# Kernel optimization log

Measured on AMD Instinct MI355X. Metric: run time of the kernel, lower is better.

## Reference

```python
import jax, jax.numpy as jnp
import numpy as np

D_MODEL = 1024
NUM_HEADS = 16
D_K = D_MODEL // NUM_HEADS


def setup_inputs() -> dict:
    key = jax.random.key(0)
    ks = jax.random.split(key, 12)
    B, S = 1, 4096
    s = 1.0 / np.sqrt(D_MODEL)
    inp = {
        'query': jax.random.normal(ks[0], (B, S, D_MODEL), jnp.float32),
        'key': jax.random.normal(ks[1], (B, S, D_MODEL), jnp.float32),
        'value': jax.random.normal(ks[2], (B, S, D_MODEL), jnp.float32),
        'W_q': jax.random.normal(ks[3], (D_MODEL, D_MODEL), jnp.float32) * s,
        'b_q': jnp.zeros((D_MODEL,), jnp.float32),
        'W_k': jax.random.normal(ks[4], (D_MODEL, D_MODEL), jnp.float32) * s,
        'b_k': jnp.zeros((D_MODEL,), jnp.float32),
        'W_v': jax.random.normal(ks[5], (D_MODEL, D_MODEL), jnp.float32) * s,
        'b_v': jnp.zeros((D_MODEL,), jnp.float32),
        'W_o': jax.random.normal(ks[6], (D_MODEL, D_MODEL), jnp.float32) * s,
        'b_o': jnp.zeros((D_MODEL,), jnp.float32),
    }
    return inp


def reference(query, key, value, W_q, b_q, W_k, b_k, W_v, b_v, W_o, b_o):
    B, S, _ = query.shape
    # torch nn.Linear: y = x @ W.T + b
    Q = query @ W_q.T + b_q
    K = key @ W_k.T + b_k
    V = value @ W_v.T + b_v
    # (B, S, H, d_k) -> (B, H, S, d_k)
    Q = Q.reshape(B, S, NUM_HEADS, D_K).transpose(0, 2, 1, 3)
    K = K.reshape(B, S, NUM_HEADS, D_K).transpose(0, 2, 1, 3)
    V = V.reshape(B, S, NUM_HEADS, D_K).transpose(0, 2, 1, 3)
    scale = 1.0 / jnp.sqrt(jnp.asarray(D_K, Q.dtype))
    qk = jnp.einsum('bhqd,bhkd->bhqk', Q, K) * scale  # [B,H,S,S]
    attn = jax.nn.softmax(qk, axis=-1)
    out = jnp.einsum('bhqk,bhkd->bhqd', attn, V)
    out = out.transpose(0, 2, 1, 3).reshape(B, S, D_MODEL)
    return out @ W_o.T + b_o
```

## Files before the change

### kernel.cpp

```cpp
#include <hip/hip_runtime.h>
#include <cstdint>
#include <cstddef>

typedef __bf16 bf16_t;
typedef _Float16 f16_t;
typedef __attribute__((ext_vector_type(8))) __bf16 bf16x8;
typedef __attribute__((ext_vector_type(4))) __bf16 bf16x4;
typedef __attribute__((ext_vector_type(2))) __bf16 bf16x2;
typedef __attribute__((ext_vector_type(8))) _Float16 f16x8;
typedef __attribute__((ext_vector_type(2))) _Float16 f16x2;
typedef __attribute__((ext_vector_type(4))) float floatx4;
typedef __attribute__((ext_vector_type(16))) float floatx16;

#define S_LEN 4096
#define DM 1024
#define NH 16
#define DKH 64
#define NSPLIT 4
#define KT_PER (S_LEN / 64 / NSPLIT)

#define QSCALE 0.1803368801111601f

__device__ __forceinline__ void async_b128(void* lds, const void* g) {
    __builtin_amdgcn_global_load_lds(
        (__attribute__((address_space(1))) void*)(uintptr_t)g,
        (__attribute__((address_space(3))) void*)lds,
        16, 0, 0);
}

__device__ __forceinline__ void fence_all() { __builtin_amdgcn_s_waitcnt(0); }

__device__ __forceinline__ floatx4 mfma16(bf16x8 a, bf16x8 b, floatx4 c) {
    return __builtin_amdgcn_mfma_f32_16x16x32_bf16(a, b, c, 0, 0, 0);
}
__device__ __forceinline__ floatx16 mfma32(bf16x8 a, bf16x8 b, floatx16 c) {
    return __builtin_amdgcn_mfma_f32_32x32x16_bf16(a, b, c, 0, 0, 0);
}
__device__ __forceinline__ int f2i(float x) { return __builtin_bit_cast(int, x); }
__device__ __forceinline__ float i2f(int x) { return __builtin_bit_cast(float, x); }
__device__ __forceinline__ int p2i(bf16x2 x) { return __builtin_bit_cast(int, x); }
__device__ __forceinline__ bf16x2 i2p(int x) { return __builtin_bit_cast(bf16x2, x); }

__global__ __launch_bounds__(256) void convert_all_kernel(
    const float* __restrict__ q, const float* __restrict__ k,
    const float* __restrict__ v, const float* __restrict__ wqf,
    const float* __restrict__ wkf, const float* __restrict__ wvf,
    const float* __restrict__ wof, bf16_t* __restrict__ dst_in,
    bf16_t* __restrict__ dst_w) {
    const size_t i = ((size_t)blockIdx.x * 256 + threadIdx.x) * 4;
    const float* s;
    bf16_t* d;
    size_t off;
    if (i < 12582912) {
        const int r = (int)(i >> 22);
        s = (r == 0) ? q : (r == 1) ? k : v;
        off = i & 4194303;
        d = dst_in + (size_t)r * 4194304 + off;
    } else {
        const size_t j = i - 12582912;
        const int r = (int)(j >> 20);
        s = (r == 0) ? wqf : (r == 1) ? wkf : (r == 2) ? wvf : wof;
        off = j & 1048575;
        d = dst_w + (size_t)r * 1048576 + off;
    }
    const floatx4 val = *(const floatx4*)(s + off);
    bf16x4 o;
    o[0] = (bf16_t)val[0]; o[1] = (bf16_t)val[1];
    o[2] = (bf16_t)val[2]; o[3] = (bf16_t)val[3];
    *(bf16x4*)d = o;
}

template <int BN, typename OutT>
__device__ __forceinline__ void gemm_bt_body(const bf16_t* __restrict__ A,
                                             const bf16_t* __restrict__ B,
                                             const float* __restrict__ bias,
                                             OutT* __restrict__ C, float oscale) {
    constexpr int K = 1024, N = 1024;
    constexpr int NT = BN / 32;
    __shared__ bf16_t As[2][128 * 32];
    __shared__ bf16_t Bs[2][BN * 32];
    const int tid = threadIdx.x;
    const int wid = tid >> 6, lane = tid & 63;
    const int quad = lane >> 4, l16 = lane & 15;
    const int m0 = blockIdx.x * 128, n0 = blockIdx.y * BN;
    const int wm = (wid & 1) * 64, wn = (wid >> 1) * (BN / 2);

    floatx4 acc[4][NT] = {};

    auto stage = [&](int buf, int k0) {
#pragma unroll
        for (int i = 0; i < 2; ++i) {
            const int c = (i << 8) + tid;
            const int row = c >> 2;
            const int ko = (c & 3) << 3;
            const int lb = ((i << 8) + (wid << 6)) << 3;
            async_b128(&As[buf][lb], A + (size_t)(m0 + row) * K + k0 + ko);
        }
#pragma unroll
        for (int i = 0; i < BN / 64; ++i) {
            const int c = (i << 8) + tid;
            const int row = c >> 2;
            const int ko = (c & 3) << 3;
            const int lb = ((i << 8) + (wid << 6)) << 3;
            async_b128(&Bs[buf][lb], B + (size_t)(n0 + row) * K + k0 + ko);
        }
    };

    stage(0, 0);
    for (int step = 0; step < K / 32; ++step) {
        const int buf = step & 1;
        fence_all();
        __syncthreads();
        if (step + 1 < K / 32) stage(buf ^ 1, (step + 1) * 32);

        bf16x8 af[4], bfr[NT];
#pragma unroll
        for (int t = 0; t < 4; ++t)
            af[t] = *(const bf16x8*)&As[buf][(wm + t * 16 + l16) * 32 + quad * 8];
#pragma unroll
        for (int t = 0; t < NT; ++t)
            bfr[t] = *(const bf16x8*)&Bs[buf][(wn + t * 16 + l16) * 32 + quad * 8];
#pragma unroll
        for (int mt = 0; mt < 4; ++mt)
#pragma unroll
            for (int nt = 0; nt < NT; ++nt)
                acc[mt][nt] = mfma16(af[mt], bfr[nt], acc[mt][nt]);
    }

#pragma unroll
    for (int mt = 0; mt < 4; ++mt)
#pragma unroll
        for (int nt = 0; nt < NT; ++nt) {
            const int col = n0 + wn + nt * 16 + l16;
            const float bv = bias[col];
#pragma unroll
            for (int r = 0; r < 4; ++r) {
                const int row = m0 + wm + mt * 16 + quad * 4 + r;
                C[(size_t)row * N + col] = (OutT)((acc[mt][nt][r] + bv) * oscale);
            }
        }
}

__global__ __launch_bounds__(256) void gemm_qkv_kernel(
    const bf16_t* __restrict__ qx, const bf16_t* __restrict__ kx,
    const bf16_t* __restrict__ vx, const bf16_t* __restrict__ wq,
    const bf16_t* __restrict__ wk, const bf16_t* __restrict__ wv,
    const float* __restrict__ bq, const float* __restrict__ bk,
    const float* __restrict__ bv, bf16_t* __restrict__ Qp,
    bf16_t* __restrict__ Kp, bf16_t* __restrict__ Vp) {
    const int z = blockIdx.z;
    const bf16_t* A = (z == 0) ? qx : (z == 1) ? kx : vx;
    const bf16_t* B = (z == 0) ? wq : (z == 1) ? wk : wv;
    const float* bias = (z == 0) ? bq : (z == 1) ? bk : bv;
    bf16_t* C = (z == 0) ? Qp : (z == 1) ? Kp : Vp;
    gemm_bt_body<128, bf16_t>(A, B, bias, C, (z == 0) ? QSCALE : 1.0f);
}

__global__ __launch_bounds__(256) void gemm_out_kernel(
    const bf16_t* __restrict__ AO, const bf16_t* __restrict__ wo,
    const float* __restrict__ bo, float* __restrict__ out) {
    gemm_bt_body<64, float>(AO, wo, bo, out, 1.0f);
}

__global__ __launch_bounds__(256) void transpose_kernel(
    const bf16_t* __restrict__ in, bf16_t* __restrict__ out) {
    __shared__ bf16_t tile[64][65];
    const int tx = threadIdx.x & 63;
    const int ty = threadIdx.x >> 6;
    const int c0 = blockIdx.x * 64;
    const int r0 = blockIdx.y * 64;
#pragma unroll
    for (int i = 0; i < 16; ++i) {
        const int r = ty + i * 4;
        tile[r][tx] = in[(size_t)(r0 + r) * DM + c0 + tx];
    }
    __syncthreads();
#pragma unroll
    for (int i = 0; i < 16; ++i) {
        const int c = ty + i * 4;
        out[(size_t)(c0 + c) * S_LEN + r0 + tx] = tile[tx][c];
    }
}

__global__ __launch_bounds__(256, 2) void flash_kernel(
    const bf16_t* __restrict__ Q, const bf16_t* __restrict__ K,
    const bf16_t* __restrict__ Vt, f16_t* __restrict__ Opart,
    float* __restrict__ Lpart) {
    __shared__ bf16_t smem[16384];
    bf16_t* Ks = smem;
    bf16_t* Vs = smem + 8192;

    const int tid = threadIdx.x;
    const int wave = tid >> 6, lane = tid & 63;
    const int h32 = lane >> 5, c = lane & 31;
    const int head = blockIdx.x;
    const int sp = blockIdx.z;
    const int qbase = blockIdx.y * 256 + wave * 64;
    const int kv0 = sp * (S_LEN / NSPLIT);

    bf16x8 Qf[2][4];
#pragma unroll
    for (int nt = 0; nt < 2; ++nt)
#pragma unroll
        for (int s = 0; s < 4; ++s)
            Qf[nt][s] = *(const bf16x8*)(Q + (size_t)(qbase + nt * 32 + c) * DM +
                                         head * DKH + s * 16 + h32 * 8);

    floatx16 oa[2][2] = {};
    floatx4 la[2] = {};

    const bf16_t* kptr = K + (size_t)(kv0 + lane) * DM + head * DKH + wave * 16;
    const bf16_t* vptr = Vt + (size_t)(head * DKH + lane) * S_LEN + kv0 + wave * 16;
    bf16_t* ksl = Ks + wave * 1024;
    bf16_t* vsl = Vs + wave * 1024;

    async_b128(ksl, kptr);       async_b128(ksl + 512, kptr + 8);
    async_b128(vsl, vptr);       async_b128(vsl + 512, vptr + 8);
    kptr += 64 * DM; vptr += 64;

    for (int kt = 0; kt < KT_PER; ++kt) {
        const int buf = kt & 1;
        fence_all();
        __syncthreads();
        if (kt + 1 < KT_PER) {
            bf16_t* kd = ksl + (buf ^ 1) * 4096;
            bf16_t* vd = vsl + (buf ^ 1) * 4096;
            async_b128(kd, kptr);     async_b128(kd + 512, kptr + 8);
            async_b128(vd, vptr);     async_b128(vd + 512, vptr + 8);
            kptr += 64 * DM; vptr += 64;
        }

        bf16x8 Kf[2][4];
#pragma unroll
        for (int mt = 0; mt < 2; ++mt)
#pragma unroll
            for (int s = 0; s < 4; ++s)
                Kf[mt][s] = *(const bf16x8*)&Ks[buf * 4096 + ((2 * s + h32) * 64 + mt * 32 + c) * 8];

        floatx16 sc[2][2] = {};
#pragma unroll
        for (int s = 0; s < 4; ++s)
#pragma unroll
            for (int mt = 0; mt < 2; ++mt)
#pragma unroll
                for (int nt = 0; nt < 2; ++nt)
                    sc[mt][nt] = mfma32(Kf[mt][s], Qf[nt][s], sc[mt][nt]);

        bf16x8 Vf[2][4];
#pragma unroll
        for (int dt = 0; dt < 2; ++dt)
#pragma unroll
            for (int s = 0; s < 4; ++s)
                Vf[dt][s] = *(const bf16x8*)&Vs[buf * 4096 + ((2 * s + h32) * 64 + dt * 32 + c) * 8];

#pragma unroll
        for (int nt = 0; nt < 2; ++nt) {
            bf16x2 pk[2][8];
#pragma unroll
            for (int mt = 0; mt < 2; ++mt)
#pragma unroll
                for (int rr = 0; rr < 8; ++rr) {
                    const float p0 = __builtin_amdgcn_exp2f(sc[mt][nt][2 * rr] - 3.0f);
                    const float p1 = __builtin_amdgcn_exp2f(sc[mt][nt][2 * rr + 1] - 3.0f);
                    la[nt][(2 * rr) & 3] += p0;
                    la[nt][(2 * rr + 1) & 3] += p1;
                    bf16x2 w; w[0] = (bf16_t)p0; w[1] = (bf16_t)p1;
                    pk[mt][rr] = w;
                }
#pragma unroll
            for (int s = 0; s < 4; ++s) {
                const int a = s >> 1, b4 = (s & 1) * 4;
                const bf16x2 r0 = h32 ? pk[a][b4 + 2] : pk[a][b4 + 0];
                const bf16x2 r1 = h32 ? pk[a][b4 + 3] : pk[a][b4 + 1];
                const bf16x2 s0 = h32 ? pk[a][b4 + 0] : pk[a][b4 + 2];
                const bf16x2 s1 = h32 ? pk[a][b4 + 1] : pk[a][b4 + 3];
                const bf16x2 x0 = i2p(__shfl_xor(p2i(s0), 32));
                const bf16x2 x1 = i2p(__shfl_xor(p2i(s1), 32));
                union { bf16x8 v; bf16x2 d[4]; } P;
                P.d[0] = h32 ? x0 : r0;
                P.d[1] = h32 ? x1 : r1;
                P.d[2] = h32 ? r0 : x0;
                P.d[3] = h32 ? r1 : x1;
                oa[0][nt] = mfma32(Vf[0][s], P.v, oa[0][nt]);
                oa[1][nt] = mfma32(Vf[1][s], P.v, oa[1][nt]);
            }
        }
    }

#pragma unroll
    for (int nt = 0; nt < 2; ++nt) {
        float t = la[nt][0] + la[nt][1] + la[nt][2] + la[nt][3];
        t += i2f(__shfl_xor(f2i(t), 32));
        if (h32 == 0)
            Lpart[(size_t)(sp * NH + head) * S_LEN + qbase + nt * 32 + c] = t;
    }

    fence_all();
    __syncthreads();
    f16_t* ot = (f16_t*)smem + wave * (32 * 72);
#pragma unroll
    for (int nt = 0; nt < 2; ++nt) {
#pragma unroll
        for (int dt = 0; dt < 2; ++dt)
#pragma unroll
            for (int rr = 0; rr < 8; ++rr) {
                const int d0 = dt * 32 + ((2 * rr) & 3) + 8 * (rr >> 1) + 4 * h32;
                f16x2 w;
                w[0] = (f16_t)oa[dt][nt][2 * rr];
                w[1] = (f16_t)oa[dt][nt][2 * rr + 1];
                *(f16x2*)&ot[c * 72 + d0] = w;
            }
        fence_all();
        __syncthreads();
        const int r = lane & 31;
#pragma unroll
        for (int j = 0; j < 4; ++j) {
            const f16x8 v = *(const f16x8*)&ot[r * 72 + h32 * 32 + j * 8];
            *(f16x8*)(Opart + ((size_t)sp * S_LEN + qbase + nt * 32 + r) * DM +
                      head * DKH + h32 * 32 + j * 8) = v;
        }
        fence_all();
        __syncthreads();
    }
}

__global__ __launch_bounds__(256) void reduce_kernel(
    const f16_t* __restrict__ Op, const float* __restrict__ Lp,
    bf16_t* __restrict__ AO) {
    const size_t f = ((size_t)blockIdx.x * 256 + threadIdx.x) * 8;
    const int q = (int)(f >> 10);
    const int h = (int)((f & 1023) >> 6);
    float l = 0.f;
#pragma unroll
    for (int sp = 0; sp < NSPLIT; ++sp)
        l += Lp[(size_t)(sp * NH + h) * S_LEN + q];
    const float inv = 1.0f / l;
    float s[8] = {};
#pragma unroll
    for (int sp = 0; sp < NSPLIT; ++sp) {
        const f16x8 v = *(const f16x8*)(Op + (size_t)sp * (S_LEN * DM) + f);
#pragma unroll
        for (int j = 0; j < 8; ++j) s[j] += (float)v[j];
    }
    bf16x8 o;
#pragma unroll
    for (int j = 0; j < 8; ++j) o[j] = (bf16_t)(s[j] * inv);
    *(bf16x8*)(AO + f) = o;
}

extern "C" void kernel_launch(void* const* d_in, const int* in_sizes, int n_in,
                              void* d_out, int out_size, void* d_ws, size_t ws_size,
                              hipStream_t stream) {
    const float* q  = (const float*)d_in[0];
    const float* k  = (const float*)d_in[1];
    const float* v  = (const float*)d_in[2];
    const float* Wq = (const float*)d_in[3];
    const float* bq = (const float*)d_in[4];
    const float* Wk = (const float*)d_in[5];
    const float* bk = (const float*)d_in[6];
    const float* Wv = (const float*)d_in[7];
    const float* bv = (const float*)d_in[8];
    const float* Wo = (const float*)d_in[9];
    const float* bo = (const float*)d_in[10];
    float* out = (float*)d_out;

    bf16_t* ws = (bf16_t*)d_ws;
    bf16_t* qx = ws;
    bf16_t* kx = qx + 4194304;
    bf16_t* vx = kx + 4194304;
    bf16_t* Vp = vx + 4194304;
    f16_t*  Opart = (f16_t*)ws;
    bf16_t* wq = Vp + 4194304;
    bf16_t* wk = wq + 1048576;
    bf16_t* wv = wk + 1048576;
    bf16_t* wo = wv + 1048576;
    bf16_t* Qp = wo + 1048576;
    bf16_t* Kp = Qp + 4194304;
    bf16_t* Vt = Kp + 4194304;
    bf16_t* AO = Vt + 4194304;
    float*  Lpart = (float*)(AO + 4194304);

    convert_all_kernel<<<dim3(16384), 256, 0, stream>>>(q, k, v, Wq, Wk, Wv, Wo,
                                                        qx, wq);
    gemm_qkv_kernel<<<dim3(32, 8, 3), 256, 0, stream>>>(qx, kx, vx, wq, wk, wv,
                                                        bq, bk, bv, Qp, Kp, Vp);
    transpose_kernel<<<dim3(16, 64), 256, 0, stream>>>(Vp, Vt);
    flash_kernel<<<dim3(16, 16, NSPLIT), 256, 0, stream>>>(Qp, Kp, Vt, Opart, Lpart);
    reduce_kernel<<<dim3(2048), 256, 0, stream>>>(Opart, Lpart, AO);
    gemm_out_kernel<<<dim3(32, 16), 256, 0, stream>>>(AO, wo, bo, out);
    (void)in_sizes; (void)n_in; (void)out_size; (void)ws_size;
}
```

Measured before the change: 284.1 us.

## Fuse V transpose into QKV GEMM epilogue and rebalance flash attention tiling

```diff
diff --git a/kernel.cpp b/kernel.cpp
--- a/kernel.cpp
+++ b/kernel.cpp
@@ -16,7 +16,7 @@
 #define DM 1024
 #define NH 16
 #define DKH 64
-#define NSPLIT 4
+#define NSPLIT 2
 #define KT_PER (S_LEN / 64 / NSPLIT)
 
 #define QSCALE 0.1803368801111601f
@@ -70,7 +70,7 @@
     *(bf16x4*)d = o;
 }
 
-template <int BN, typename OutT>
+template <int BN, typename OutT, bool TR>
 __device__ __forceinline__ void gemm_bt_body(const bf16_t* __restrict__ A,
                                              const bf16_t* __restrict__ B,
                                              const float* __restrict__ bias,
@@ -133,10 +133,19 @@
         for (int nt = 0; nt < NT; ++nt) {
             const int col = n0 + wn + nt * 16 + l16;
             const float bv = bias[col];
-#pragma unroll
-            for (int r = 0; r < 4; ++r) {
-                const int row = m0 + wm + mt * 16 + quad * 4 + r;
-                C[(size_t)row * N + col] = (OutT)((acc[mt][nt][r] + bv) * oscale);
+            if (TR) {
+                bf16x4 o4;
+#pragma unroll
+                for (int r = 0; r < 4; ++r)
+                    o4[r] = (bf16_t)((acc[mt][nt][r] + bv) * oscale);
+                *(bf16x4*)((bf16_t*)C + (size_t)col * S_LEN +
+                           (m0 + wm + mt * 16 + quad * 4)) = o4;
+            } else {
+#pragma unroll
+                for (int r = 0; r < 4; ++r) {
+                    const int row = m0 + wm + mt * 16 + quad * 4 + r;
+                    C[(size_t)row * N + col] = (OutT)((acc[mt][nt][r] + bv) * oscale);
+                }
             }
         }
 }
@@ -146,40 +155,24 @@
     const bf16_t* __restrict__ vx, const bf16_t* __restrict__ wq,
     const bf16_t* __restrict__ wk, const bf16_t* __restrict__ wv,
     const float* __restrict__ bq, const float* __restrict__ bk,
-    const float* __restrict__ bv, bf16_t* __restrict__ Qp,
-    bf16_t* __restrict__ Kp, bf16_t* __restrict__ Vp) {
+    const float* __restrict__ bvv, bf16_t* __restrict__ Qp,
+    bf16_t* __restrict__ Kp, bf16_t* __restrict__ Vt) {
     const int z = blockIdx.z;
-    const bf16_t* A = (z == 0) ? qx : (z == 1) ? kx : vx;
-    const bf16_t* B = (z == 0) ? wq : (z == 1) ? wk : wv;
-    const float* bias = (z == 0) ? bq : (z == 1) ? bk : bv;
-    bf16_t* C = (z == 0) ? Qp : (z == 1) ? Kp : Vp;
-    gemm_bt_body<128, bf16_t>(A, B, bias, C, (z == 0) ? QSCALE : 1.0f);
+    if (z == 2) {
+        gemm_bt_body<128, bf16_t, true>(vx, wv, bvv, Vt, 1.0f);
+    } else {
+        const bf16_t* A = (z == 0) ? qx : kx;
+        const bf16_t* B = (z == 0) ? wq : wk;
+        const float* bias = (z == 0) ? bq : bk;
+        bf16_t* C = (z == 0) ? Qp : Kp;
+        gemm_bt_body<128, bf16_t, false>(A, B, bias, C, (z == 0) ? QSCALE : 1.0f);
+    }
 }
 
 __global__ __launch_bounds__(256) void gemm_out_kernel(
     const bf16_t* __restrict__ AO, const bf16_t* __restrict__ wo,
     const float* __restrict__ bo, float* __restrict__ out) {
-    gemm_bt_body<64, float>(AO, wo, bo, out, 1.0f);
-}
-
-__global__ __launch_bounds__(256) void transpose_kernel(
-    const bf16_t* __restrict__ in, bf16_t* __restrict__ out) {
-    __shared__ bf16_t tile[64][65];
-    const int tx = threadIdx.x & 63;
-    const int ty = threadIdx.x >> 6;
-    const int c0 = blockIdx.x * 64;
-    const int r0 = blockIdx.y * 64;
-#pragma unroll
-    for (int i = 0; i < 16; ++i) {
-        const int r = ty + i * 4;
-        tile[r][tx] = in[(size_t)(r0 + r) * DM + c0 + tx];
-    }
-    __syncthreads();
-#pragma unroll
-    for (int i = 0; i < 16; ++i) {
-        const int c = ty + i * 4;
-        out[(size_t)(c0 + c) * S_LEN + r0 + tx] = tile[tx][c];
-    }
+    gemm_bt_body<64, float, false>(AO, wo, bo, out, 1.0f);
 }
 
 __global__ __launch_bounds__(256, 2) void flash_kernel(
@@ -195,19 +188,17 @@
     const int h32 = lane >> 5, c = lane & 31;
     const int head = blockIdx.x;
     const int sp = blockIdx.z;
-    const int qbase = blockIdx.y * 256 + wave * 64;
+    const int qbase = blockIdx.y * 128 + wave * 32;
     const int kv0 = sp * (S_LEN / NSPLIT);
 
-    bf16x8 Qf[2][4];
-#pragma unroll
-    for (int nt = 0; nt < 2; ++nt)
-#pragma unroll
-        for (int s = 0; s < 4; ++s)
-            Qf[nt][s] = *(const bf16x8*)(Q + (size_t)(qbase + nt * 32 + c) * DM +
-                                         head * DKH + s * 16 + h32 * 8);
-
-    floatx16 oa[2][2] = {};
-    floatx4 la[2] = {};
+    bf16x8 Qf[4];
+#pragma unroll
+    for (int s = 0; s < 4; ++s)
+        Qf[s] = *(const bf16x8*)(Q + (size_t)(qbase + c) * DM +
+                                 head * DKH + s * 16 + h32 * 8);
+
+    floatx16 oa[2] = {};
+    floatx4 la = {};
 
     const bf16_t* kptr = K + (size_t)(kv0 + lane) * DM + head * DKH + wave * 16;
     const bf16_t* vptr = Vt + (size_t)(head * DKH + lane) * S_LEN + kv0 + wave * 16;
@@ -237,14 +228,12 @@
             for (int s = 0; s < 4; ++s)
                 Kf[mt][s] = *(const bf16x8*)&Ks[buf * 4096 + ((2 * s + h32) * 64 + mt * 32 + c) * 8];
 
-        floatx16 sc[2][2] = {};
+        floatx16 sc[2] = {};
 #pragma unroll
         for (int s = 0; s < 4; ++s)
 #pragma unroll
             for (int mt = 0; mt < 2; ++mt)
-#pragma unroll
-                for (int nt = 0; nt < 2; ++nt)
-                    sc[mt][nt] = mfma32(Kf[mt][s], Qf[nt][s], sc[mt][nt]);
+                sc[mt] = mfma32(Kf[mt][s], Qf[s], sc[mt]);
 
         bf16x8 Vf[2][4];
 #pragma unroll
@@ -253,74 +242,67 @@
             for (int s = 0; s < 4; ++s)
                 Vf[dt][s] = *(const bf16x8*)&Vs[buf * 4096 + ((2 * s + h32) * 64 + dt * 32 + c) * 8];
 
-#pragma unroll
-        for (int nt = 0; nt < 2; ++nt) {
-            bf16x2 pk[2][8];
-#pragma unroll
-            for (int mt = 0; mt < 2; ++mt)
-#pragma unroll
-                for (int rr = 0; rr < 8; ++rr) {
-                    const float p0 = __builtin_amdgcn_exp2f(sc[mt][nt][2 * rr] - 3.0f);
-                    const float p1 = __builtin_amdgcn_exp2f(sc[mt][nt][2 * rr + 1] - 3.0f);
-                    la[nt][(2 * rr) & 3] += p0;
-                    la[nt][(2 * rr + 1) & 3] += p1;
-                    bf16x2 w; w[0] = (bf16_t)p0; w[1] = (bf16_t)p1;
-                    pk[mt][rr] = w;
-                }
-#pragma unroll
-            for (int s = 0; s < 4; ++s) {
-                const int a = s >> 1, b4 = (s & 1) * 4;
-                const bf16x2 r0 = h32 ? pk[a][b4 + 2] : pk[a][b4 + 0];
-                const bf16x2 r1 = h32 ? pk[a][b4 + 3] : pk[a][b4 + 1];
-                const bf16x2 s0 = h32 ? pk[a][b4 + 0] : pk[a][b4 + 2];
-                const bf16x2 s1 = h32 ? pk[a][b4 + 1] : pk[a][b4 + 3];
-                const bf16x2 x0 = i2p(__shfl_xor(p2i(s0), 32));
-                const bf16x2 x1 = i2p(__shfl_xor(p2i(s1), 32));
-                union { bf16x8 v; bf16x2 d[4]; } P;
-                P.d[0] = h32 ? x0 : r0;
-                P.d[1] = h32 ? x1 : r1;
-                P.d[2] = h32 ? r0 : x0;
-                P.d[3] = h32 ? r1 : x1;
-                oa[0][nt] = mfma32(Vf[0][s], P.v, oa[0][nt]);
-                oa[1][nt] = mfma32(Vf[1][s], P.v, oa[1][nt]);
+        bf16x2 pk[2][8];
+#pragma unroll
+        for (int mt = 0; mt < 2; ++mt)
+#pragma unroll
+            for (int rr = 0; rr < 8; ++rr) {
+                const float p0 = __builtin_amdgcn_exp2f(sc[mt][2 * rr] - 3.0f);
+                const float p1 = __builtin_amdgcn_exp2f(sc[mt][2 * rr + 1] - 3.0f);
+                la[(2 * rr) & 3] += p0;
+                la[(2 * rr + 1) & 3] += p1;
+                bf16x2 w; w[0] = (bf16_t)p0; w[1] = (bf16_t)p1;
+                pk[mt][rr] = w;
             }
-        }
-    }
-
-#pragma unroll
-    for (int nt = 0; nt < 2; ++nt) {
-        float t = la[nt][0] + la[nt][1] + la[nt][2] + la[nt][3];
+#pragma unroll
+        for (int s = 0; s < 4; ++s) {
+            const int a = s >> 1, b4 = (s & 1) * 4;
+            const bf16x2 r0 = h32 ? pk[a][b4 + 2] : pk[a][b4 + 0];
+            const bf16x2 r1 = h32 ? pk[a][b4 + 3] : pk[a][b4 + 1];
+            const bf16x2 s0 = h32 ? pk[a][b4 + 0] : pk[a][b4 + 2];
+            const bf16x2 s1 = h32 ? pk[a][b4 + 1] : pk[a][b4 + 3];
+            const bf16x2 x0 = i2p(__shfl_xor(p2i(s0), 32));
+            const bf16x2 x1 = i2p(__shfl_xor(p2i(s1), 32));
+            union { bf16x8 v; bf16x2 d[4]; } P;
+            P.d[0] = h32 ? x0 : r0;
+            P.d[1] = h32 ? x1 : r1;
+            P.d[2] = h32 ? r0 : x0;
+            P.d[3] = h32 ? r1 : x1;
+            oa[0] = mfma32(Vf[0][s], P.v, oa[0]);
+            oa[1] = mfma32(Vf[1][s], P.v, oa[1]);
+        }
+    }
+
+    {
+        float t = la[0] + la[1] + la[2] + la[3];
         t += i2f(__shfl_xor(f2i(t), 32));
         if (h32 == 0)
-            Lpart[(size_t)(sp * NH + head) * S_LEN + qbase + nt * 32 + c] = t;
+            Lpart[(size_t)(sp * NH + head) * S_LEN + qbase + c] = t;
     }
 
     fence_all();
     __syncthreads();
     f16_t* ot = (f16_t*)smem + wave * (32 * 72);
 #pragma unroll
-    for (int nt = 0; nt < 2; ++nt) {
-#pragma unroll
-        for (int dt = 0; dt < 2; ++dt)
-#pragma unroll
-            for (int rr = 0; rr < 8; ++rr) {
-                const int d0 = dt * 32 + ((2 * rr) & 3) + 8 * (rr >> 1) + 4 * h32;
-                f16x2 w;
-                w[0] = (f16_t)oa[dt][nt][2 * rr];
-                w[1] = (f16_t)oa[dt][nt][2 * rr + 1];
-                *(f16x2*)&ot[c * 72 + d0] = w;
-            }
-        fence_all();
-        __syncthreads();
+    for (int dt = 0; dt < 2; ++dt)
+#pragma unroll
+        for (int rr = 0; rr < 8; ++rr) {
+            const int d0 = dt * 32 + ((2 * rr) & 3) + 8 * (rr >> 1) + 4 * h32;
+            f16x2 w;
+            w[0] = (f16_t)oa[dt][2 * rr];
+            w[1] = (f16_t)oa[dt][2 * rr + 1];
+            *(f16x2*)&ot[c * 72 + d0] = w;
+        }
+    fence_all();
+    __syncthreads();
+    {
         const int r = lane & 31;
 #pragma unroll
         for (int j = 0; j < 4; ++j) {
             const f16x8 v = *(const f16x8*)&ot[r * 72 + h32 * 32 + j * 8];
-            *(f16x8*)(Opart + ((size_t)sp * S_LEN + qbase + nt * 32 + r) * DM +
+            *(f16x8*)(Opart + ((size_t)sp * S_LEN + qbase + r) * DM +
                       head * DKH + h32 * 32 + j * 8) = v;
         }
-        fence_all();
-        __syncthreads();
     }
 }
 
@@ -368,9 +350,8 @@
     bf16_t* qx = ws;
     bf16_t* kx = qx + 4194304;
     bf16_t* vx = kx + 4194304;
-    bf16_t* Vp = vx + 4194304;
     f16_t*  Opart = (f16_t*)ws;
-    bf16_t* wq = Vp + 4194304;
+    bf16_t* wq = ws + 16777216;
     bf16_t* wk = wq + 1048576;
     bf16_t* wv = wk + 1048576;
     bf16_t* wo = wv + 1048576;
@@ -383,9 +364,8 @@
     convert_all_kernel<<<dim3(16384), 256, 0, stream>>>(q, k, v, Wq, Wk, Wv, Wo,
                                                         qx, wq);
     gemm_qkv_kernel<<<dim3(32, 8, 3), 256, 0, stream>>>(qx, kx, vx, wq, wk, wv,
-                                                        bq, bk, bv, Qp, Kp, Vp);
-    transpose_kernel<<<dim3(16, 64), 256, 0, stream>>>(Vp, Vt);
-    flash_kernel<<<dim3(16, 16, NSPLIT), 256, 0, stream>>>(Qp, Kp, Vt, Opart, Lpart);
+                                                        bq, bk, bv, Qp, Kp, Vt);
+    flash_kernel<<<dim3(16, 32, NSPLIT), 256, 0, stream>>>(Qp, Kp, Vt, Opart, Lpart);
     reduce_kernel<<<dim3(2048), 256, 0, stream>>>(Opart, Lpart, AO);
     gemm_out_kernel<<<dim3(32, 16), 256, 0, stream>>>(AO, wo, bo, out);
     (void)in_sizes; (void)n_in; (void)out_size; (void)ws_size;
```

Measured after the change: 290.3 us. 1.02x slower.
